# Kernel optimization log

Measured on AMD Instinct MI355X. Metric: run time of the kernel, lower is better.

Reference implementation:

```python
import jax, jax.numpy as jnp
import numpy as np
from jax.ops import segment_sum

N = 50000
E = 800000
D_IN = 128
D_H = 64
D_OUT = 1
NUM_GRAPHS = 64


def setup_inputs() -> dict:
    key = jax.random.key(0)
    ks = jax.random.split(key, 12)
    x = jax.random.normal(ks[0], (N, D_IN), dtype=jnp.float32)
    edge_index = jax.random.randint(ks[1], (2, E), 0, N, dtype=jnp.int32)
    batch = jnp.sort(jax.random.randint(ks[2], (N,), 0, NUM_GRAPHS, dtype=jnp.int32))
    def glorot(k, fan_in, fan_out):
        lim = np.sqrt(6.0 / (fan_in + fan_out))
        return jax.random.uniform(k, (fan_in, fan_out), jnp.float32, -lim, lim)
    return {
        "x": x,
        "edge_index": edge_index,
        "batch": batch,
        "W1": glorot(ks[3], D_IN, D_H), "b1": jnp.zeros((D_H,), jnp.float32),
        "W2": glorot(ks[4], D_H, D_H), "b2": jnp.zeros((D_H,), jnp.float32),
        "W3": glorot(ks[5], D_H, D_H), "b3": jnp.zeros((D_H,), jnp.float32),
        "Wl": glorot(ks[6], D_H, D_OUT), "bl": jnp.zeros((D_OUT,), jnp.float32),
    }


def _gcn_conv(x, W, b, row, col, norm):
    # x' = scatter_add(norm * (xW)[row] -> col) + b   (PyG GCNConv with self-loops)
    h = x @ W                                   # [N, d_out]
    msg = h[row] * norm[:, None]                # [E+N, d_out] gather + scale
    out = segment_sum(msg, col, num_segments=N) # scatter-add at targets
    return out + b


def reference(x, edge_index, batch, W1, b1, W2, b2, W3, b3, Wl, bl):
    # add self loops
    loops = jnp.arange(N, dtype=edge_index.dtype)
    row = jnp.concatenate([edge_index[0], loops])  # sources
    col = jnp.concatenate([edge_index[1], loops])  # targets
    # symmetric degree normalization (degree over targets, incl. self loops)
    deg = segment_sum(jnp.ones_like(col, dtype=x.dtype), col, num_segments=N)
    dinv = jnp.where(deg > 0, jax.lax.rsqrt(deg), 0.0)
    norm = dinv[row] * dinv[col]

    h = jax.nn.elu(_gcn_conv(x, W1, b1, row, col, norm))
    h = jax.nn.elu(_gcn_conv(h, W2, b2, row, col, norm))
    h = jax.nn.elu(_gcn_conv(h, W3, b3, row, col, norm))
    h = h @ Wl + bl                                         # [N, 1]
    # global mean pool over graphs
    sums = segment_sum(h, batch, num_segments=NUM_GRAPHS)   # [G, 1]
    cnts = segment_sum(jnp.ones((N, 1), h.dtype), batch, num_segments=NUM_GRAPHS)
    pooled = sums / jnp.maximum(cnts, 1.0)
    return jnp.squeeze(pooled)
```

## Files before the change

kernel.cpp:

```cpp
#include <hip/hip_runtime.h>
#include <math.h>

#define NN 50000
#define NE 800000
#define DIN 128
#define DH 64
#define NG 64

#define GEMM_BLOCKS ((NN + 63) / 64)
#define DEG_BLOCKS 2048
#define FILL_BLOCKS 2048
#define SCAN_BLOCKS ((NN + 255) / 256)

template <int K>
__global__ __launch_bounds__(256, 4) void gemm_deg_kernel(const float* __restrict__ in,
                                                          const float* __restrict__ W,
                                                          float* __restrict__ out, int n,
                                                          const int* __restrict__ col,
                                                          int* __restrict__ indeg, int e) {
    __shared__ float Ws[K * 64];
    if (blockIdx.x >= GEMM_BLOCKS) {
        int i = (blockIdx.x - GEMM_BLOCKS) * 256 + threadIdx.x;
        int stride = DEG_BLOCKS * 256;
        for (; i < e; i += stride) atomicAdd(&indeg[col[i]], 1);
        return;
    }
    for (int t = threadIdx.x; t < K * 16; t += 256)
        reinterpret_cast<float4*>(Ws)[t] = reinterpret_cast<const float4*>(W)[t];
    __syncthreads();

    int w = threadIdx.x >> 6, l = threadIdx.x & 63;
    int fq = l & 15;
    int nl = l >> 4;
    int base = blockIdx.x * 64 + w * 16 + nl * 4;

    const float* r0 = in + (size_t)min(base + 0, n - 1) * K;
    const float* r1 = in + (size_t)min(base + 1, n - 1) * K;
    const float* r2 = in + (size_t)min(base + 2, n - 1) * K;
    const float* r3 = in + (size_t)min(base + 3, n - 1) * K;

    float acc[4][4];
    #pragma unroll
    for (int i = 0; i < 4; ++i)
        #pragma unroll
        for (int f = 0; f < 4; ++f) acc[i][f] = 0.f;

    #pragma unroll 2
    for (int k = 0; k < K; k += 4) {
        float4 wv[4];
        #pragma unroll
        for (int kk = 0; kk < 4; ++kk)
            wv[kk] = *reinterpret_cast<const float4*>(&Ws[(k + kk) * 64 + 4 * fq]);
        float4 xv[4];
        xv[0] = *reinterpret_cast<const float4*>(r0 + k);
        xv[1] = *reinterpret_cast<const float4*>(r1 + k);
        xv[2] = *reinterpret_cast<const float4*>(r2 + k);
        xv[3] = *reinterpret_cast<const float4*>(r3 + k);
        #pragma unroll
        for (int i = 0; i < 4; ++i) {
            float xs[4] = {xv[i].x, xv[i].y, xv[i].z, xv[i].w};
            #pragma unroll
            for (int kk = 0; kk < 4; ++kk) {
                acc[i][0] = fmaf(xs[kk], wv[kk].x, acc[i][0]);
                acc[i][1] = fmaf(xs[kk], wv[kk].y, acc[i][1]);
                acc[i][2] = fmaf(xs[kk], wv[kk].z, acc[i][2]);
                acc[i][3] = fmaf(xs[kk], wv[kk].w, acc[i][3]);
            }
        }
    }

    #pragma unroll
    for (int i = 0; i < 4; ++i) {
        int node = base + i;
        if (node < n) {
            float4 o = make_float4(acc[i][0], acc[i][1], acc[i][2], acc[i][3]);
            *reinterpret_cast<float4*>(&out[(size_t)node * 64 + 4 * fq]) = o;
        }
    }
}

template <int K>
__global__ __launch_bounds__(256, 4) void gemm_kernel(const float* __restrict__ in,
                                                      const float* __restrict__ W,
                                                      float* __restrict__ out, int n) {
    __shared__ float Ws[K * 64];
    for (int t = threadIdx.x; t < K * 16; t += 256)
        reinterpret_cast<float4*>(Ws)[t] = reinterpret_cast<const float4*>(W)[t];
    __syncthreads();

    int w = threadIdx.x >> 6, l = threadIdx.x & 63;
    int fq = l & 15;
    int nl = l >> 4;
    int base = blockIdx.x * 64 + w * 16 + nl * 4;

    const float* r0 = in + (size_t)min(base + 0, n - 1) * K;
    const float* r1 = in + (size_t)min(base + 1, n - 1) * K;
    const float* r2 = in + (size_t)min(base + 2, n - 1) * K;
    const float* r3 = in + (size_t)min(base + 3, n - 1) * K;

    float acc[4][4];
    #pragma unroll
    for (int i = 0; i < 4; ++i)
        #pragma unroll
        for (int f = 0; f < 4; ++f) acc[i][f] = 0.f;

    #pragma unroll 2
    for (int k = 0; k < K; k += 4) {
        float4 wv[4];
        #pragma unroll
        for (int kk = 0; kk < 4; ++kk)
            wv[kk] = *reinterpret_cast<const float4*>(&Ws[(k + kk) * 64 + 4 * fq]);
        float4 xv[4];
        xv[0] = *reinterpret_cast<const float4*>(r0 + k);
        xv[1] = *reinterpret_cast<const float4*>(r1 + k);
        xv[2] = *reinterpret_cast<const float4*>(r2 + k);
        xv[3] = *reinterpret_cast<const float4*>(r3 + k);
        #pragma unroll
        for (int i = 0; i < 4; ++i) {
            float xs[4] = {xv[i].x, xv[i].y, xv[i].z, xv[i].w};
            #pragma unroll
            for (int kk = 0; kk < 4; ++kk) {
                acc[i][0] = fmaf(xs[kk], wv[kk].x, acc[i][0]);
                acc[i][1] = fmaf(xs[kk], wv[kk].y, acc[i][1]);
                acc[i][2] = fmaf(xs[kk], wv[kk].z, acc[i][2]);
                acc[i][3] = fmaf(xs[kk], wv[kk].w, acc[i][3]);
            }
        }
    }

    #pragma unroll
    for (int i = 0; i < 4; ++i) {
        int node = base + i;
        if (node < n) {
            float4 o = make_float4(acc[i][0], acc[i][1], acc[i][2], acc[i][3]);
            *reinterpret_cast<float4*>(&out[(size_t)node * 64 + 4 * fq]) = o;
        }
    }
}

__global__ __launch_bounds__(256) void scan_phaseA(const int* __restrict__ indeg,
                                                   int* __restrict__ partial, int n) {
    int i = blockIdx.x * 256 + threadIdx.x;
    int v = (i < n) ? indeg[i] : 0;
    int s = v;
    #pragma unroll
    for (int d = 1; d < 64; d <<= 1) s += __shfl_xor(s, d, 64);
    __shared__ int ws[4];
    if ((threadIdx.x & 63) == 0) ws[threadIdx.x >> 6] = s;
    __syncthreads();
    if (threadIdx.x == 0) partial[blockIdx.x] = ws[0] + ws[1] + ws[2] + ws[3];
}

__global__ __launch_bounds__(256) void scan_phaseB(int* __restrict__ partial, int nb) {
    int t = threadIdx.x;
    int lane = t & 63, wid = t >> 6;
    int v = (t < nb) ? partial[t] : 0;
    int inc = v;
    #pragma unroll
    for (int d = 1; d < 64; d <<= 1) {
        int u = __shfl_up(inc, d, 64);
        if (lane >= d) inc += u;
    }
    __shared__ int ws[4];
    if (lane == 63) ws[wid] = inc;
    __syncthreads();
    int woff = 0;
    #pragma unroll
    for (int k = 0; k < 4; ++k) woff += (k < wid) ? ws[k] : 0;
    if (t < nb) partial[t] = woff + inc - v;
}

__global__ __launch_bounds__(256) void scan_phaseC(const int* __restrict__ indeg,
                                                   const int* __restrict__ partial,
                                                   int* __restrict__ off,
                                                   int* __restrict__ cursor,
                                                   float* __restrict__ dinv, int n) {
    int i = blockIdx.x * 256 + threadIdx.x;
    int d = (i < n) ? indeg[i] : 0;
    int lane = threadIdx.x & 63, wid = threadIdx.x >> 6;
    int inc = d;
    #pragma unroll
    for (int dd = 1; dd < 64; dd <<= 1) {
        int u = __shfl_up(inc, dd, 64);
        if (lane >= dd) inc += u;
    }
    __shared__ int ws[4];
    if (lane == 63) ws[wid] = inc;
    __syncthreads();
    int woff = 0;
    #pragma unroll
    for (int k = 0; k < 4; ++k) woff += (k < wid) ? ws[k] : 0;
    int excl = partial[blockIdx.x] + woff + inc - d;
    if (i < n) {
        off[i] = excl;
        cursor[i] = excl;
        dinv[i] = rsqrtf((float)(d + 1));
        if (i == n - 1) off[n] = excl + d;
    }
}

__global__ void fill_kernel(const int* __restrict__ row, const int* __restrict__ col,
                            const float* __restrict__ dinv, int* __restrict__ cursor,
                            float2* __restrict__ ew, int e) {
    int i = blockIdx.x * blockDim.x + threadIdx.x;
    int stride = gridDim.x * blockDim.x;
    for (; i < e; i += stride) {
        int c = col[i], r = row[i];
        int p = atomicAdd(&cursor[c], 1);
        ew[p] = make_float2(__int_as_float(r), dinv[r] * dinv[c]);
    }
}

__global__ __launch_bounds__(256) void pull_kernel(const float* __restrict__ tmp,
                                                   const int* __restrict__ off,
                                                   const float2* __restrict__ ew,
                                                   const float* __restrict__ dinv,
                                                   const float* __restrict__ bias,
                                                   float* __restrict__ out, int n) {
    int wid = threadIdx.x >> 6;
    int lane = threadIdx.x & 63;
    int node = blockIdx.x * 4 + wid;
    if (node >= n) return;
    int fg = lane & 15, e4 = lane >> 4;
    const float4* trow = reinterpret_cast<const float4*>(tmp);

    float4 acc = make_float4(0.f, 0.f, 0.f, 0.f);
    int e = off[node], s1 = off[node + 1];

    for (; e + 8 <= s1; e += 8) {
        float2 m0 = ew[e + e4];
        float2 m1 = ew[e + 4 + e4];
        float4 v0 = trow[(size_t)__float_as_int(m0.x) * 16 + fg];
        float4 v1 = trow[(size_t)__float_as_int(m1.x) * 16 + fg];
        acc.x = fmaf(v0.x, m0.y, acc.x);
        acc.y = fmaf(v0.y, m0.y, acc.y);
        acc.z = fmaf(v0.z, m0.y, acc.z);
        acc.w = fmaf(v0.w, m0.y, acc.w);
        acc.x = fmaf(v1.x, m1.y, acc.x);
        acc.y = fmaf(v1.y, m1.y, acc.y);
        acc.z = fmaf(v1.z, m1.y, acc.z);
        acc.w = fmaf(v1.w, m1.y, acc.w);
    }
    for (; e < s1; e += 4) {
        int idx = e + e4;
        if (idx < s1) {
            float2 m = ew[idx];
            float4 v = trow[(size_t)__float_as_int(m.x) * 16 + fg];
            acc.x = fmaf(v.x, m.y, acc.x);
            acc.y = fmaf(v.y, m.y, acc.y);
            acc.z = fmaf(v.z, m.y, acc.z);
            acc.w = fmaf(v.w, m.y, acc.w);
        }
    }

    acc.x += __shfl_xor(acc.x, 16, 64);
    acc.y += __shfl_xor(acc.y, 16, 64);
    acc.z += __shfl_xor(acc.z, 16, 64);
    acc.w += __shfl_xor(acc.w, 16, 64);
    acc.x += __shfl_xor(acc.x, 32, 64);
    acc.y += __shfl_xor(acc.y, 32, 64);
    acc.z += __shfl_xor(acc.z, 32, 64);
    acc.w += __shfl_xor(acc.w, 32, 64);

    float dt = dinv[node];
    float s2 = dt * dt;
    float4 self = trow[(size_t)node * 16 + fg];
    float4 b4 = reinterpret_cast<const float4*>(bias)[fg];
    float4 r;
    r.x = acc.x + self.x * s2 + b4.x;
    r.y = acc.y + self.y * s2 + b4.y;
    r.z = acc.z + self.z * s2 + b4.z;
    r.w = acc.w + self.w * s2 + b4.w;
    r.x = (r.x > 0.f) ? r.x : expm1f(r.x);
    r.y = (r.y > 0.f) ? r.y : expm1f(r.y);
    r.z = (r.z > 0.f) ? r.z : expm1f(r.z);
    r.w = (r.w > 0.f) ? r.w : expm1f(r.w);
    if (e4 == 0)
        reinterpret_cast<float4*>(out)[(size_t)node * 16 + fg] = r;
}

#define POOL_BLOCKS 256
__global__ __launch_bounds__(256) void final_pool_kernel(const float* __restrict__ h,
                                                         const float* __restrict__ Wl,
                                                         const int* __restrict__ batch,
                                                         float* __restrict__ gsum,
                                                         float* __restrict__ gcnt, int n) {
    __shared__ float lsum[NG];
    __shared__ float lcnt[NG];
    if (threadIdx.x < NG) { lsum[threadIdx.x] = 0.f; lcnt[threadIdx.x] = 0.f; }
    __syncthreads();
    int wid = threadIdx.x >> 6, lane = threadIdx.x & 63;
    float wl = Wl[lane];
    int per_block = (n + POOL_BLOCKS - 1) / POOL_BLOCKS;
    int start = blockIdx.x * per_block;
    int end = start + per_block;
    if (end > n) end = n;
    for (int node = start + wid; node < end; node += 4) {
        float p = h[(size_t)node * 64 + lane] * wl;
        #pragma unroll
        for (int d = 32; d >= 1; d >>= 1) p += __shfl_xor(p, d, 64);
        if (lane == 0) {
            int g = batch[node];
            atomicAdd(&lsum[g], p);
            atomicAdd(&lcnt[g], 1.f);
        }
    }
    __syncthreads();
    if (threadIdx.x < NG && lcnt[threadIdx.x] != 0.f) {
        atomicAdd(&gsum[threadIdx.x], lsum[threadIdx.x]);
        atomicAdd(&gcnt[threadIdx.x], lcnt[threadIdx.x]);
    }
}

__global__ void pool_div_kernel(const float* __restrict__ gsum, const float* __restrict__ gcnt,
                                const float* __restrict__ bl, float* __restrict__ out) {
    int g = threadIdx.x;
    if (g < NG) {
        float c = gcnt[g];
        out[g] = (c > 0.5f) ? (gsum[g] / c + bl[0]) : 0.f;
    }
}

extern "C" void kernel_launch(void* const* d_in, const int* in_sizes, int n_in,
                              void* d_out, int out_size, void* d_ws, size_t ws_size,
                              hipStream_t stream) {
    const float* x    = (const float*)d_in[0];
    const int*   eidx = (const int*)d_in[1];
    const int*   row  = eidx;
    const int*   col  = eidx + NE;
    const int*   batch = (const int*)d_in[2];
    const float* W1 = (const float*)d_in[3];
    const float* b1 = (const float*)d_in[4];
    const float* W2 = (const float*)d_in[5];
    const float* b2 = (const float*)d_in[6];
    const float* W3 = (const float*)d_in[7];
    const float* b3 = (const float*)d_in[8];
    const float* Wl = (const float*)d_in[9];
    const float* bl = (const float*)d_in[10];
    float* out = (float*)d_out;

    size_t cur = 0;
    auto take = [&](size_t elems) { size_t c = cur; cur += (elems + 63) & ~(size_t)63; return c; };
    float* base_f = (float*)d_ws;
    int*   base_i = (int*)d_ws;

    float*  dinv    = base_f + take(NN);
    int*    indeg   = base_i + take(NN);
    int*    csr_off = base_i + take(NN + 1);
    int*    cursor  = base_i + take(NN);
    int*    partial = base_i + take(SCAN_BLOCKS);
    float2* ew      = (float2*)(base_f + take((size_t)NE * 2));
    float*  tmp     = base_f + take((size_t)NN * 64);
    float*  h       = base_f + take((size_t)NN * 64);
    float*  gg      = base_f + take(2 * NG);
    float*  gsum    = gg;
    float*  gcnt    = gg + NG;
    (void)ws_size; (void)n_in; (void)in_sizes; (void)out_size;

    hipMemsetAsync(indeg, 0, NN * sizeof(int), stream);
    hipMemsetAsync(gg, 0, 2 * NG * sizeof(float), stream);

    const int nblk_pull = (NN + 3) / 4;

    gemm_deg_kernel<DIN><<<GEMM_BLOCKS + DEG_BLOCKS, 256, 0, stream>>>(
        x, W1, tmp, NN, col, indeg, NE);
    scan_phaseA<<<SCAN_BLOCKS, 256, 0, stream>>>(indeg, partial, NN);
    scan_phaseB<<<1, 256, 0, stream>>>(partial, SCAN_BLOCKS);
    scan_phaseC<<<SCAN_BLOCKS, 256, 0, stream>>>(indeg, partial, csr_off, cursor, dinv, NN);
    fill_kernel<<<FILL_BLOCKS, 256, 0, stream>>>(row, col, dinv, cursor, ew, NE);

    pull_kernel<<<nblk_pull, 256, 0, stream>>>(tmp, csr_off, ew, dinv, b1, h, NN);

    gemm_kernel<DH><<<GEMM_BLOCKS, 256, 0, stream>>>(h, W2, tmp, NN);
    pull_kernel<<<nblk_pull, 256, 0, stream>>>(tmp, csr_off, ew, dinv, b2, h, NN);

    gemm_kernel<DH><<<GEMM_BLOCKS, 256, 0, stream>>>(h, W3, tmp, NN);
    pull_kernel<<<nblk_pull, 256, 0, stream>>>(tmp, csr_off, ew, dinv, b3, h, NN);

    final_pool_kernel<<<POOL_BLOCKS, 256, 0, stream>>>(h, Wl, batch, gsum, gcnt, NN);
    pool_div_kernel<<<1, 64, 0, stream>>>(gsum, gcnt, bl, out);
}
```

Before: 333.7 us.

## Fuse first GEMM with CSR fill instead of degree count; vectorize degree kernel

Moves the first-layer GEMM so it runs together with the CSR fill pass, and puts the degree counting in its own kernel that reads col as int4. The fill now stores only dinv[row] per edge, and the pull kernel multiplies the accumulated sum by the target's dinv once per node. The aim is to overlap the GEMM with the atomic-heavy fill, which is the longer scatter phase, and to cut per-edge multiplies. In exchange the degree kernel becomes a separate launch that is no longer overlapped with anything.

```diff
diff --git a/kernel.cpp b/kernel.cpp
--- a/kernel.cpp
+++ b/kernel.cpp
@@ -8,21 +8,41 @@
 #define NG 64
 
 #define GEMM_BLOCKS ((NN + 63) / 64)
-#define DEG_BLOCKS 2048
+#define DEG_BLOCKS 1024
 #define FILL_BLOCKS 2048
 #define SCAN_BLOCKS ((NN + 255) / 256)
 
+__global__ __launch_bounds__(256) void deg_kernel(const int4* __restrict__ col4,
+                                                  int* __restrict__ indeg, int e4) {
+    int i = blockIdx.x * 256 + threadIdx.x;
+    int stride = gridDim.x * 256;
+    for (; i < e4; i += stride) {
+        int4 c = col4[i];
+        atomicAdd(&indeg[c.x], 1);
+        atomicAdd(&indeg[c.y], 1);
+        atomicAdd(&indeg[c.z], 1);
+        atomicAdd(&indeg[c.w], 1);
+    }
+}
+
 template <int K>
-__global__ __launch_bounds__(256, 4) void gemm_deg_kernel(const float* __restrict__ in,
-                                                          const float* __restrict__ W,
-                                                          float* __restrict__ out, int n,
-                                                          const int* __restrict__ col,
-                                                          int* __restrict__ indeg, int e) {
+__global__ __launch_bounds__(256, 4) void gemm_fill_kernel(const float* __restrict__ in,
+                                                           const float* __restrict__ W,
+                                                           float* __restrict__ out, int n,
+                                                           const int* __restrict__ row,
+                                                           const int* __restrict__ col,
+                                                           const float* __restrict__ dinv,
+                                                           int* __restrict__ cursor,
+                                                           float2* __restrict__ ew, int e) {
     __shared__ float Ws[K * 64];
     if (blockIdx.x >= GEMM_BLOCKS) {
         int i = (blockIdx.x - GEMM_BLOCKS) * 256 + threadIdx.x;
-        int stride = DEG_BLOCKS * 256;
-        for (; i < e; i += stride) atomicAdd(&indeg[col[i]], 1);
+        int stride = FILL_BLOCKS * 256;
+        for (; i < e; i += stride) {
+            int c = col[i], r = row[i];
+            int p = atomicAdd(&cursor[c], 1);
+            ew[p] = make_float2(__int_as_float(r), dinv[r]);
+        }
         return;
     }
     for (int t = threadIdx.x; t < K * 16; t += 256)
@@ -196,18 +216,6 @@
         cursor[i] = excl;
         dinv[i] = rsqrtf((float)(d + 1));
         if (i == n - 1) off[n] = excl + d;
-    }
-}
-
-__global__ void fill_kernel(const int* __restrict__ row, const int* __restrict__ col,
-                            const float* __restrict__ dinv, int* __restrict__ cursor,
-                            float2* __restrict__ ew, int e) {
-    int i = blockIdx.x * blockDim.x + threadIdx.x;
-    int stride = gridDim.x * blockDim.x;
-    for (; i < e; i += stride) {
-        int c = col[i], r = row[i];
-        int p = atomicAdd(&cursor[c], 1);
-        ew[p] = make_float2(__int_as_float(r), dinv[r] * dinv[c]);
     }
 }
 
@@ -267,10 +275,10 @@
     float4 self = trow[(size_t)node * 16 + fg];
     float4 b4 = reinterpret_cast<const float4*>(bias)[fg];
     float4 r;
-    r.x = acc.x + self.x * s2 + b4.x;
-    r.y = acc.y + self.y * s2 + b4.y;
-    r.z = acc.z + self.z * s2 + b4.z;
-    r.w = acc.w + self.w * s2 + b4.w;
+    r.x = fmaf(acc.x, dt, fmaf(self.x, s2, b4.x));
+    r.y = fmaf(acc.y, dt, fmaf(self.y, s2, b4.y));
+    r.z = fmaf(acc.z, dt, fmaf(self.z, s2, b4.z));
+    r.w = fmaf(acc.w, dt, fmaf(self.w, s2, b4.w));
     r.x = (r.x > 0.f) ? r.x : expm1f(r.x);
     r.y = (r.y > 0.f) ? r.y : expm1f(r.y);
     r.z = (r.z > 0.f) ? r.z : expm1f(r.z);
@@ -362,12 +370,13 @@
 
     const int nblk_pull = (NN + 3) / 4;
 
-    gemm_deg_kernel<DIN><<<GEMM_BLOCKS + DEG_BLOCKS, 256, 0, stream>>>(
-        x, W1, tmp, NN, col, indeg, NE);
+    deg_kernel<<<DEG_BLOCKS, 256, 0, stream>>>(
+        reinterpret_cast<const int4*>(col), indeg, NE / 4);
     scan_phaseA<<<SCAN_BLOCKS, 256, 0, stream>>>(indeg, partial, NN);
     scan_phaseB<<<1, 256, 0, stream>>>(partial, SCAN_BLOCKS);
     scan_phaseC<<<SCAN_BLOCKS, 256, 0, stream>>>(indeg, partial, csr_off, cursor, dinv, NN);
-    fill_kernel<<<FILL_BLOCKS, 256, 0, stream>>>(row, col, dinv, cursor, ew, NE);
+    gemm_fill_kernel<DIN><<<GEMM_BLOCKS + FILL_BLOCKS, 256, 0, stream>>>(
+        x, W1, tmp, NN, row, col, dinv, cursor, ew, NE);
 
     pull_kernel<<<nblk_pull, 256, 0, stream>>>(tmp, csr_off, ew, dinv, b1, h, NN);
 
```

Result: slower. 342.8 us (+2.7%).

## Factor symmetric GCN normalization into row prescale and target postscale, drop edge weights

Applied to the files above, without the earlier changes.

Rewrites norm = dinv[r]*dinv[c] by prescaling the transformed features by the source dinv (in the GEMM epilogue, or in a separate scale pass for layer 1) and multiplying the aggregated sum by the target dinv in the pull kernel. The CSR edge array then stores only source indices instead of (index, weight) pairs. This halves edge metadata traffic in all three pull passes and removes the dinv gathers in the fill kernel. The cost is an extra read-modify-write pass over the 50000x64 layer-1 tmp, which runs concurrently with the fill blocks.

```diff
diff --git a/kernel.cpp b/kernel.cpp
--- a/kernel.cpp
+++ b/kernel.cpp
@@ -10,6 +10,7 @@
 #define GEMM_BLOCKS ((NN + 63) / 64)
 #define DEG_BLOCKS 2048
 #define FILL_BLOCKS 2048
+#define SCALE_BLOCKS 256
 #define SCAN_BLOCKS ((NN + 255) / 256)
 
 template <int K>
@@ -80,9 +81,10 @@
 }
 
 template <int K>
-__global__ __launch_bounds__(256, 4) void gemm_kernel(const float* __restrict__ in,
-                                                      const float* __restrict__ W,
-                                                      float* __restrict__ out, int n) {
+__global__ __launch_bounds__(256, 4) void gemm_scaled_kernel(const float* __restrict__ in,
+                                                             const float* __restrict__ W,
+                                                             const float* __restrict__ dinv,
+                                                             float* __restrict__ out, int n) {
     __shared__ float Ws[K * 64];
     for (int t = threadIdx.x; t < K * 16; t += 256)
         reinterpret_cast<float4*>(Ws)[t] = reinterpret_cast<const float4*>(W)[t];
@@ -132,7 +134,9 @@
     for (int i = 0; i < 4; ++i) {
         int node = base + i;
         if (node < n) {
-            float4 o = make_float4(acc[i][0], acc[i][1], acc[i][2], acc[i][3]);
+            float sc = dinv[node];
+            float4 o = make_float4(acc[i][0] * sc, acc[i][1] * sc,
+                                   acc[i][2] * sc, acc[i][3] * sc);
             *reinterpret_cast<float4*>(&out[(size_t)node * 64 + 4 * fq]) = o;
         }
     }
@@ -199,21 +203,37 @@
     }
 }
 
-__global__ void fill_kernel(const int* __restrict__ row, const int* __restrict__ col,
-                            const float* __restrict__ dinv, int* __restrict__ cursor,
-                            float2* __restrict__ ew, int e) {
-    int i = blockIdx.x * blockDim.x + threadIdx.x;
-    int stride = gridDim.x * blockDim.x;
-    for (; i < e; i += stride) {
-        int c = col[i], r = row[i];
-        int p = atomicAdd(&cursor[c], 1);
-        ew[p] = make_float2(__int_as_float(r), dinv[r] * dinv[c]);
+__global__ __launch_bounds__(256) void fill_scale_kernel(const int* __restrict__ row,
+                                                         const int* __restrict__ col,
+                                                         int* __restrict__ cursor,
+                                                         int* __restrict__ ews, int e,
+                                                         float* __restrict__ tmp,
+                                                         const float* __restrict__ dinv,
+                                                         int n4) {
+    if (blockIdx.x < FILL_BLOCKS) {
+        int i = blockIdx.x * 256 + threadIdx.x;
+        int stride = FILL_BLOCKS * 256;
+        for (; i < e; i += stride) {
+            int c = col[i];
+            int p = atomicAdd(&cursor[c], 1);
+            ews[p] = row[i];
+        }
+    } else {
+        float4* t4 = reinterpret_cast<float4*>(tmp);
+        int i = (blockIdx.x - FILL_BLOCKS) * 256 + threadIdx.x;
+        int stride = SCALE_BLOCKS * 256;
+        for (; i < n4; i += stride) {
+            float sc = dinv[i >> 4];
+            float4 v = t4[i];
+            v.x *= sc; v.y *= sc; v.z *= sc; v.w *= sc;
+            t4[i] = v;
+        }
     }
 }
 
 __global__ __launch_bounds__(256) void pull_kernel(const float* __restrict__ tmp,
                                                    const int* __restrict__ off,
-                                                   const float2* __restrict__ ew,
+                                                   const int* __restrict__ ews,
                                                    const float* __restrict__ dinv,
                                                    const float* __restrict__ bias,
                                                    float* __restrict__ out, int n) {
@@ -228,28 +248,23 @@
     int e = off[node], s1 = off[node + 1];
 
     for (; e + 8 <= s1; e += 8) {
-        float2 m0 = ew[e + e4];
-        float2 m1 = ew[e + 4 + e4];
-        float4 v0 = trow[(size_t)__float_as_int(m0.x) * 16 + fg];
-        float4 v1 = trow[(size_t)__float_as_int(m1.x) * 16 + fg];
-        acc.x = fmaf(v0.x, m0.y, acc.x);
-        acc.y = fmaf(v0.y, m0.y, acc.y);
-        acc.z = fmaf(v0.z, m0.y, acc.z);
-        acc.w = fmaf(v0.w, m0.y, acc.w);
-        acc.x = fmaf(v1.x, m1.y, acc.x);
-        acc.y = fmaf(v1.y, m1.y, acc.y);
-        acc.z = fmaf(v1.z, m1.y, acc.z);
-        acc.w = fmaf(v1.w, m1.y, acc.w);
+        int i0 = ews[e + e4];
+        int i1 = ews[e + 4 + e4];
+        float4 v0 = trow[(size_t)i0 * 16 + fg];
+        float4 v1 = trow[(size_t)i1 * 16 + fg];
+        acc.x += v0.x + v1.x;
+        acc.y += v0.y + v1.y;
+        acc.z += v0.z + v1.z;
+        acc.w += v0.w + v1.w;
     }
     for (; e < s1; e += 4) {
         int idx = e + e4;
         if (idx < s1) {
-            float2 m = ew[idx];
-            float4 v = trow[(size_t)__float_as_int(m.x) * 16 + fg];
-            acc.x = fmaf(v.x, m.y, acc.x);
-            acc.y = fmaf(v.y, m.y, acc.y);
-            acc.z = fmaf(v.z, m.y, acc.z);
-            acc.w = fmaf(v.w, m.y, acc.w);
+            float4 v = trow[(size_t)ews[idx] * 16 + fg];
+            acc.x += v.x;
+            acc.y += v.y;
+            acc.z += v.z;
+            acc.w += v.w;
         }
     }
 
@@ -263,14 +278,13 @@
     acc.w += __shfl_xor(acc.w, 32, 64);
 
     float dt = dinv[node];
-    float s2 = dt * dt;
     float4 self = trow[(size_t)node * 16 + fg];
     float4 b4 = reinterpret_cast<const float4*>(bias)[fg];
     float4 r;
-    r.x = acc.x + self.x * s2 + b4.x;
-    r.y = acc.y + self.y * s2 + b4.y;
-    r.z = acc.z + self.z * s2 + b4.z;
-    r.w = acc.w + self.w * s2 + b4.w;
+    r.x = fmaf(acc.x + self.x, dt, b4.x);
+    r.y = fmaf(acc.y + self.y, dt, b4.y);
+    r.z = fmaf(acc.z + self.z, dt, b4.z);
+    r.w = fmaf(acc.w + self.w, dt, b4.w);
     r.x = (r.x > 0.f) ? r.x : expm1f(r.x);
     r.y = (r.y > 0.f) ? r.y : expm1f(r.y);
     r.z = (r.z > 0.f) ? r.z : expm1f(r.z);
@@ -349,7 +363,7 @@
     int*    csr_off = base_i + take(NN + 1);
     int*    cursor  = base_i + take(NN);
     int*    partial = base_i + take(SCAN_BLOCKS);
-    float2* ew      = (float2*)(base_f + take((size_t)NE * 2));
+    int*    ews     = base_i + take(NE);
     float*  tmp     = base_f + take((size_t)NN * 64);
     float*  h       = base_f + take((size_t)NN * 64);
     float*  gg      = base_f + take(2 * NG);
@@ -367,15 +381,16 @@
     scan_phaseA<<<SCAN_BLOCKS, 256, 0, stream>>>(indeg, partial, NN);
     scan_phaseB<<<1, 256, 0, stream>>>(partial, SCAN_BLOCKS);
     scan_phaseC<<<SCAN_BLOCKS, 256, 0, stream>>>(indeg, partial, csr_off, cursor, dinv, NN);
-    fill_kernel<<<FILL_BLOCKS, 256, 0, stream>>>(row, col, dinv, cursor, ew, NE);
-
-    pull_kernel<<<nblk_pull, 256, 0, stream>>>(tmp, csr_off, ew, dinv, b1, h, NN);
-
-    gemm_kernel<DH><<<GEMM_BLOCKS, 256, 0, stream>>>(h, W2, tmp, NN);
-    pull_kernel<<<nblk_pull, 256, 0, stream>>>(tmp, csr_off, ew, dinv, b2, h, NN);
-
-    gemm_kernel<DH><<<GEMM_BLOCKS, 256, 0, stream>>>(h, W3, tmp, NN);
-    pull_kernel<<<nblk_pull, 256, 0, stream>>>(tmp, csr_off, ew, dinv, b3, h, NN);
+    fill_scale_kernel<<<FILL_BLOCKS + SCALE_BLOCKS, 256, 0, stream>>>(
+        row, col, cursor, ews, NE, tmp, dinv, NN * 16);
+
+    pull_kernel<<<nblk_pull, 256, 0, stream>>>(tmp, csr_off, ews, dinv, b1, h, NN);
+
+    gemm_scaled_kernel<DH><<<GEMM_BLOCKS, 256, 0, stream>>>(h, W2, dinv, tmp, NN);
+    pull_kernel<<<nblk_pull, 256, 0, stream>>>(tmp, csr_off, ews, dinv, b2, h, NN);
+
+    gemm_scaled_kernel<DH><<<GEMM_BLOCKS, 256, 0, stream>>>(h, W3, dinv, tmp, NN);
+    pull_kernel<<<nblk_pull, 256, 0, stream>>>(tmp, csr_off, ews, dinv, b3, h, NN);
 
     final_pool_kernel<<<POOL_BLOCKS, 256, 0, stream>>>(h, Wl, batch, gsum, gcnt, NN);
     pool_div_kernel<<<1, 64, 0, stream>>>(gsum, gcnt, bl, out);
```

Result: slower. 341.0 us (+2.2%).
